# Kernel optimization log

Measured on AMD Instinct MI355X. Metric: run time of the kernel, lower is better.

## Reference

```python
import jax, jax.numpy as jnp
import numpy as np
import math

HIDDEN, HEADS, D_K = 768, 12, 64
BS, SEQ = 4, 2048


def setup_inputs() -> dict:
    key = jax.random.key(0)
    ks = jax.random.split(key, 5)
    s = 1.0 / math.sqrt(HIDDEN)
    return {
        "x": jax.random.normal(ks[0], (BS, SEQ, HIDDEN), dtype=jnp.float32),
        "Wq": jax.random.normal(ks[1], (HIDDEN, HIDDEN), dtype=jnp.float32) * s,
        "bq": jnp.zeros((HIDDEN,), jnp.float32),
        "Wk": jax.random.normal(ks[2], (HIDDEN, HIDDEN), dtype=jnp.float32) * s,
        "bk": jnp.zeros((HIDDEN,), jnp.float32),
        "Wv": jax.random.normal(ks[3], (HIDDEN, HIDDEN), dtype=jnp.float32) * s,
        "bv": jnp.zeros((HIDDEN,), jnp.float32),
        "Wo": jax.random.normal(ks[4], (HIDDEN, HIDDEN), dtype=jnp.float32) * s,
        "bo": jnp.zeros((HIDDEN,), jnp.float32),
    }


def reference(x, Wq, bq, Wk, bk, Wv, bv, Wo, bo):
    bs, seq, _ = x.shape
    # projections; nn.Linear computes x @ W.T + b
    def proj(W, b):
        y = jnp.einsum("bsd,ed->bse", x, W) + b
        return y.reshape(bs, seq, HEADS, D_K).transpose(0, 2, 1, 3)  # [b,h,s,d]
    q, k, v = proj(Wq, bq), proj(Wk, bk), proj(Wv, bv)
    scores = jnp.einsum("bhqd,bhkd->bhqk", q, k) / jnp.sqrt(jnp.float32(D_K))
    attn = jax.nn.softmax(scores, axis=-1)  # dropout = 0 (eval)
    ctx = jnp.einsum("bhqk,bhkd->bhqd", attn, v)
    ctx = ctx.transpose(0, 2, 1, 3).reshape(bs, seq, HIDDEN)
    return jnp.einsum("bsd,ed->bse", ctx, Wo) + bo
```

## Files before the change

kernel.cpp:

```cpp
#include <hip/hip_runtime.h>
#include <hip/hip_bf16.h>

#define HID 768
#define NHEAD 12
#define DKH 64
#define BSZ 4
#define SEQ 2048
#define MTOT (BSZ*SEQ)
#define NBH (BSZ*NHEAD)

typedef __attribute__((ext_vector_type(8))) short   s16x8;
typedef __attribute__((ext_vector_type(8))) __bf16  bf16x8;
typedef __attribute__((ext_vector_type(4))) __bf16  bf16x4;
typedef __attribute__((ext_vector_type(4))) float   f32x4;

#define MFMA16x32(A,B,C) __builtin_amdgcn_mfma_f32_16x16x32_bf16((A),(B),(C),0,0,0)

__device__ __forceinline__ unsigned short f2bf(float f) {
  union { float f; unsigned int u; } a; a.f = f;
  return (unsigned short)((a.u + 0x7FFFu + ((a.u >> 16) & 1u)) >> 16);
}

__device__ __forceinline__ void gload_lds16(const unsigned short* g, unsigned short* l) {
  __builtin_amdgcn_global_load_lds((const __attribute__((address_space(1))) void*)g,
                                   (__attribute__((address_space(3))) void*)l, 16, 0, 0);
}

__global__ __launch_bounds__(256) void cvt_kernel(const float* __restrict__ src,
                                                  unsigned short* __restrict__ dst, int n) {
  int i = (blockIdx.x * 256 + threadIdx.x) * 4;
  if (i >= n) return;
  float4 v = *(const float4*)(src + i);
  ushort4 o;
  o.x = f2bf(v.x); o.y = f2bf(v.y); o.z = f2bf(v.z); o.w = f2bf(v.w);
  *(ushort4*)(dst + i) = o;
}

__global__ __launch_bounds__(256) void cvtw_kernel(const float* __restrict__ s0,
                                                   const float* __restrict__ s1,
                                                   const float* __restrict__ s2,
                                                   const float* __restrict__ s3,
                                                   unsigned short* __restrict__ dst) {
  const float* s = (blockIdx.y == 0) ? s0 : (blockIdx.y == 1) ? s1 : (blockIdx.y == 2) ? s2 : s3;
  int i = (blockIdx.x * 256 + threadIdx.x) * 4;
  float4 v = *(const float4*)(s + i);
  ushort4 o;
  o.x = f2bf(v.x); o.y = f2bf(v.y); o.z = f2bf(v.z); o.w = f2bf(v.w);
  *(ushort4*)(dst + (size_t)blockIdx.y * HID * HID + i) = o;
}

template<int MODE>
__global__ __launch_bounds__(256) void gemm_kernel(
    const unsigned short* __restrict__ A,
    const unsigned short* __restrict__ W,
    const float* __restrict__ bias0,
    const float* __restrict__ bias1,
    const float* __restrict__ bias2,
    void* __restrict__ out_raw,
    unsigned short* __restrict__ vtimg)
{
  __shared__ unsigned short As[128*64];
  __shared__ unsigned short Bs[128*64];
  const int tid  = threadIdx.x;
  const int wave = tid >> 6, lane = tid & 63;
  const int l16  = lane & 15, lg = lane >> 4;
  const int f    = blockIdx.x;
  const int xcd  = f & 7, rr = f >> 3;
  const int bx   = xcd*8 + (rr & 7), by = rr >> 3;
  const int m0   = bx * 128, n0 = by * 128;
  const int wm   = (wave & 1) * 64,  wn = (wave >> 1) * 64;

  const f32x4 z4 = {0.f, 0.f, 0.f, 0.f};
  f32x4 acc[4][4];
#pragma unroll
  for (int i = 0; i < 4; ++i)
#pragma unroll
    for (int j = 0; j < 4; ++j) acc[i][j] = z4;

  const int sr  = lane >> 3;
  const int sc8 = ((lane & 7) ^ sr) << 3;

  for (int kt = 0; kt < HID; kt += 64) {
    __syncthreads();
#pragma unroll
    for (int i = 0; i < 4; ++i) {
      const int c = wave * 4 + i;
      gload_lds16(A + (size_t)(m0 + c*8 + sr) * HID + kt + sc8, As + c*512);
      gload_lds16(W + (size_t)(n0 + c*8 + sr) * HID + kt + sc8, Bs + c*512);
    }
    __syncthreads();
    const char* ab = (const char*)As;
    const char* bb = (const char*)Bs;
#pragma unroll
    for (int kk = 0; kk < 2; ++kk) {
      bf16x8 af[4], bfr[4];
#pragma unroll
      for (int mb = 0; mb < 4; ++mb) {
        const int r = wm + mb*16 + l16;
        af[mb] = *(const bf16x8*)(ab + r*128 + (((kk*4 + lg) ^ (l16 & 7)) << 4));
      }
#pragma unroll
      for (int nb = 0; nb < 4; ++nb) {
        const int r = wn + nb*16 + l16;
        bfr[nb] = *(const bf16x8*)(bb + r*128 + (((kk*4 + lg) ^ (l16 & 7)) << 4));
      }
#pragma unroll
      for (int mb = 0; mb < 4; ++mb)
#pragma unroll
        for (int nb = 0; nb < 4; ++nb)
          acc[mb][nb] = MFMA16x32(af[mb], bfr[nb], acc[mb][nb]);
    }
  }

  if (MODE == 0) {
    unsigned short* out = (unsigned short*)out_raw;
    const float QSCALE = 0.18033688011112042f;
    const int which = (n0 + wn) / HID;
    if (which == 2) {
      const int h = (n0 + wn - 2*HID) >> 6;
#pragma unroll
      for (int nb = 0; nb < 4; ++nb) {
        const int d = nb*16 + l16;
        const float bias = bias2[h*64 + d];
#pragma unroll
        for (int mb = 0; mb < 4; ++mb) {
          const int m    = m0 + wm + mb*16 + lg*4;
          const int b    = m >> 11, s = m & (SEQ - 1);
          const int tile = s >> 6;
          const int slot = ((s & 63) >> 2) ^ l16;
          ushort4 w;
          w.x = f2bf(acc[mb][nb][0] + bias);
          w.y = f2bf(acc[mb][nb][1] + bias);
          w.z = f2bf(acc[mb][nb][2] + bias);
          w.w = f2bf(acc[mb][nb][3] + bias);
          *(ushort4*)(vtimg + ((((size_t)(b*NHEAD + h)*32 + tile)*64 + d)*64 + slot*4)) = w;
        }
      }
    } else {
      const float* bp  = (which == 0) ? bias0 : bias1;
      const float scl  = (which == 0) ? QSCALE : 1.0f;
      const int e_base = n0 + wn - which*HID;
#pragma unroll
      for (int nb = 0; nb < 4; ++nb) {
        const int e = e_base + nb*16 + l16;
        const float bias = bp[e];
        const int h = e >> 6, d = e & 63;
#pragma unroll
        for (int mb = 0; mb < 4; ++mb)
#pragma unroll
          for (int j = 0; j < 4; ++j) {
            const int m = m0 + wm + mb*16 + lg*4 + j;
            const int b = m >> 11, s = m & (SEQ - 1);
            const float v = (acc[mb][nb][j] + bias) * scl;
            out[((((size_t)which*BSZ + b)*NHEAD + h)*SEQ + s)*DKH + d] = f2bf(v);
          }
      }
    }
  } else {
    float* out = (float*)out_raw;
#pragma unroll
    for (int nb = 0; nb < 4; ++nb) {
      const int n = n0 + wn + nb*16 + l16;
      const float bias = bias0[n];
#pragma unroll
      for (int mb = 0; mb < 4; ++mb)
#pragma unroll
        for (int j = 0; j < 4; ++j) {
          const int m = m0 + wm + mb*16 + lg*4 + j;
          out[(size_t)m*HID + n] = acc[mb][nb][j] + bias;
        }
    }
  }
}

#define ATTN_STEP(CUR, DOPREF)                                              \
  {                                                                         \
    if (DOPREF) {                                                           \
      gload_lds16(kSrc0, Ks[(CUR)^1] + wave*1024);                          \
      gload_lds16(kSrc1, Ks[(CUR)^1] + wave*1024 + 512);                    \
      gload_lds16(vSrc0, Vs[(CUR)^1] + wave*1024);                          \
      gload_lds16(vSrc1, Vs[(CUR)^1] + wave*1024 + 512);                    \
      kSrc0 += 64*DKH; kSrc1 += 64*DKH; vSrc0 += 4096; vSrc1 += 4096;       \
    }                                                                       \
    const char* kb = (const char*)Ks[CUR];                                  \
    const char* vb = (const char*)Vs[CUR];                                  \
    f32x4 sc[2][4];                                                         \
    __builtin_amdgcn_s_setprio(1);                                          \
    _Pragma("unroll")                                                       \
    for (int nb = 0; nb < 4; ++nb) {                                        \
      bf16x8 kf0 = *(const bf16x8*)(kb + kbase0 + nb*2048);                 \
      bf16x8 kf1 = *(const bf16x8*)(kb + kbase1 + nb*2048);                 \
      f32x4 z0 = z4, z1 = z4;                                               \
      z0 = MFMA16x32(kf0, qf[0][0], z0);                                    \
      z0 = MFMA16x32(kf1, qf[0][1], z0);                                    \
      z1 = MFMA16x32(kf0, qf[1][0], z1);                                    \
      z1 = MFMA16x32(kf1, qf[1][1], z1);                                    \
      sc[0][nb] = z0; sc[1][nb] = z1;                                       \
    }                                                                       \
    __builtin_amdgcn_s_setprio(0);                                          \
    bf16x8 pa[2][2];                                                        \
    _Pragma("unroll")                                                       \
    for (int qa = 0; qa < 2; ++qa)                                          \
      _Pragma("unroll")                                                     \
      for (int nb = 0; nb < 4; ++nb)                                        \
        _Pragma("unroll")                                                   \
        for (int j = 0; j < 4; ++j)                                         \
          pa[qa][nb>>1][(nb&1)*4 + j] =                                     \
            (__bf16)__builtin_amdgcn_exp2f(sc[qa][nb][j]);                  \
    __builtin_amdgcn_s_setprio(1);                                          \
    csum[0] = MFMA16x32(pa[0][0], ones, csum[0]);                           \
    csum[0] = MFMA16x32(pa[0][1], ones, csum[0]);                           \
    csum[1] = MFMA16x32(pa[1][0], ones, csum[1]);                           \
    csum[1] = MFMA16x32(pa[1][1], ones, csum[1]);                           \
    _Pragma("unroll")                                                       \
    for (int db = 0; db < 4; ++db) {                                        \
      bf16x4 v00 = *(const bf16x4*)(vb + vbase0 + db*2048);                 \
      bf16x4 v01 = *(const bf16x4*)(vb + vbase1 + db*2048);                 \
      bf16x4 v10 = *(const bf16x4*)(vb + vbase2 + db*2048);                 \
      bf16x4 v11 = *(const bf16x4*)(vb + vbase3 + db*2048);                 \
      bf16x8 vf0 = __builtin_shufflevector(v00, v01, 0,1,2,3,4,5,6,7);      \
      bf16x8 vf1 = __builtin_shufflevector(v10, v11, 0,1,2,3,4,5,6,7);      \
      cacc[0][db] = MFMA16x32(pa[0][0], vf0, cacc[0][db]);                  \
      cacc[0][db] = MFMA16x32(pa[0][1], vf1, cacc[0][db]);                  \
      cacc[1][db] = MFMA16x32(pa[1][0], vf0, cacc[1][db]);                  \
      cacc[1][db] = MFMA16x32(pa[1][1], vf1, cacc[1][db]);                  \
    }                                                                       \
    __builtin_amdgcn_s_setprio(0);                                          \
    __syncthreads();                                                        \
  }

__global__ __launch_bounds__(256, 3) void attn_kernel(const unsigned short* __restrict__ qkv,
                                                      const unsigned short* __restrict__ vtimg,
                                                      unsigned short* __restrict__ ctx)
{
  __shared__ unsigned short Ks[2][64*64];
  __shared__ unsigned short Vs[2][64*64];
  const int tid  = threadIdx.x;
  const int wave = tid >> 6, lane = tid & 63;
  const int l16  = lane & 15, lg = lane >> 4;
  const int f   = blockIdx.x;
  const int xcd = f & 7, idx = f >> 3;
  const int bh  = xcd * 6 + (idx >> 4);
  const int qt  = idx & 15;
  const int b   = bh / NHEAD, h = bh - b * NHEAD;
  const int q0  = qt * 128 + wave * 32;

  const unsigned short* Qg = qkv + (size_t)bh * (SEQ*DKH);
  const unsigned short* Kg = qkv + (size_t)(NBH + bh) * (SEQ*DKH);

  const int srow  = lane >> 3;
  const int scolK = ((lane & 7) ^ srow) << 3;
  const unsigned short* kSrc0 = Kg + (size_t)(wave*16 + srow) * DKH + scolK;
  const unsigned short* kSrc1 = Kg + (size_t)(wave*16 + 8 + srow) * DKH + scolK;
  const unsigned short* vSrc0 = vtimg + ((size_t)bh*32*64 + wave*16 + srow) * 64 + (lane & 7) * 8;
  const unsigned short* vSrc1 = vSrc0 + 8*64;

  const int kbase0 = l16*128 + ((lg ^ (l16 & 7)) << 4);
  const int kbase1 = l16*128 + (((lg + 4) ^ (l16 & 7)) << 4);
  const int vbase0 = l16*128 + (((lg     ) ^ l16) << 3);
  const int vbase1 = l16*128 + (((lg +  4) ^ l16) << 3);
  const int vbase2 = l16*128 + (((lg +  8) ^ l16) << 3);
  const int vbase3 = l16*128 + (((lg + 12) ^ l16) << 3);

  bf16x8 qf[2][2];
#pragma unroll
  for (int qa = 0; qa < 2; ++qa) {
    qf[qa][0] = *(const bf16x8*)(Qg + (size_t)(q0 + qa*16 + l16)*DKH + lg*8);
    qf[qa][1] = *(const bf16x8*)(Qg + (size_t)(q0 + qa*16 + l16)*DKH + 32 + lg*8);
  }

  bf16x8 ones;
#pragma unroll
  for (int e = 0; e < 8; ++e) ones[e] = (__bf16)1.0f;

  const f32x4 z4 = {0.f,0.f,0.f,0.f};
  f32x4 cacc[2][4];
  f32x4 csum[2] = {z4, z4};
#pragma unroll
  for (int qa = 0; qa < 2; ++qa)
#pragma unroll
    for (int db = 0; db < 4; ++db) cacc[qa][db] = z4;

  gload_lds16(kSrc0, Ks[0] + wave*1024);
  gload_lds16(kSrc1, Ks[0] + wave*1024 + 512);
  gload_lds16(vSrc0, Vs[0] + wave*1024);
  gload_lds16(vSrc1, Vs[0] + wave*1024 + 512);
  kSrc0 += 64*DKH; kSrc1 += 64*DKH; vSrc0 += 4096; vSrc1 += 4096;
  __syncthreads();

#pragma unroll 1
  for (int tt = 0; tt < 16; ++tt) {
    ATTN_STEP(0, true)
    ATTN_STEP(1, (tt < 15))
  }

#pragma unroll
  for (int qa = 0; qa < 2; ++qa) {
    f32x4 inv;
#pragma unroll
    for (int j = 0; j < 4; ++j) inv[j] = 1.0f / csum[qa][j];
#pragma unroll
    for (int db = 0; db < 4; ++db)
#pragma unroll
      for (int j = 0; j < 4; ++j) {
        const int srow2 = q0 + qa*16 + lg*4 + j;
        ctx[((size_t)(b*SEQ + srow2))*HID + h*DKH + db*16 + l16] = f2bf(cacc[qa][db][j] * inv[j]);
      }
  }
}

extern "C" void kernel_launch(void* const* d_in, const int* in_sizes, int n_in,
                              void* d_out, int out_size, void* d_ws, size_t ws_size,
                              hipStream_t stream) {
  (void)in_sizes; (void)n_in; (void)out_size; (void)ws_size;
  const float* x  = (const float*)d_in[0];
  const float* Wq = (const float*)d_in[1];
  const float* bq = (const float*)d_in[2];
  const float* Wk = (const float*)d_in[3];
  const float* bk = (const float*)d_in[4];
  const float* Wv = (const float*)d_in[5];
  const float* bv = (const float*)d_in[6];
  const float* Wo = (const float*)d_in[7];
  const float* bo = (const float*)d_in[8];

  unsigned short* ws   = (unsigned short*)d_ws;
  unsigned short* Xb   = ws;
  unsigned short* Wqkv = Xb + (size_t)MTOT * HID;
  unsigned short* Wob  = Wqkv + (size_t)3 * HID * HID;
  unsigned short* qkvb = Wob + (size_t)HID * HID;
  unsigned short* vtb  = qkvb + (size_t)2 * NBH * SEQ * DKH;
  unsigned short* ctxb = Xb;

  cvt_kernel<<<(MTOT*HID)/1024, 256, 0, stream>>>(x, Xb, MTOT*HID);
  cvtw_kernel<<<dim3((HID*HID)/1024, 4), 256, 0, stream>>>(Wq, Wk, Wv, Wo, Wqkv);

  gemm_kernel<0><<<1152, 256, 0, stream>>>(Xb, Wqkv, bq, bk, bv, qkvb, vtb);
  attn_kernel<<<768, 256, 0, stream>>>(qkvb, vtb, ctxb);
  gemm_kernel<1><<<384, 256, 0, stream>>>(ctxb, Wob, bo, nullptr, nullptr, d_out, nullptr);
}
```

Before: 135.3 us.

## Double-buffer GEMM LDS tiles to overlap global loads with MFMA compute

The GEMM kernel now keeps two LDS buffers for the A and W tiles. It issues the global-to-LDS loads for the next K tile before computing on the current one, with one barrier per step instead of two. This is meant to hide global memory latency behind MFMA work. The cost is doubled LDS use (64KB per block), which may reduce occupancy. Correctness also depends on the global_load_lds completing before the barrier that follows.

```diff
diff --git a/kernel.cpp b/kernel.cpp
--- a/kernel.cpp
+++ b/kernel.cpp
@@ -49,6 +49,42 @@
   *(ushort4*)(dst + (size_t)blockIdx.y * HID * HID + i) = o;
 }
 
+#define GEMM_STEP(CUR, KTN, DOPREF)                                         \
+  {                                                                         \
+    if (DOPREF) {                                                           \
+      _Pragma("unroll")                                                     \
+      for (int i = 0; i < 4; ++i) {                                         \
+        const int c = wave * 4 + i;                                         \
+        gload_lds16(Aptr + (size_t)(c*8 + sr) * HID + (KTN) + sc8,          \
+                    As[(CUR)^1] + c*512);                                   \
+        gload_lds16(Wptr + (size_t)(c*8 + sr) * HID + (KTN) + sc8,          \
+                    Bs[(CUR)^1] + c*512);                                   \
+      }                                                                     \
+    }                                                                       \
+    const char* ab = (const char*)As[CUR];                                  \
+    const char* bb = (const char*)Bs[CUR];                                  \
+    _Pragma("unroll")                                                       \
+    for (int kk = 0; kk < 2; ++kk) {                                        \
+      bf16x8 af[4], bfr[4];                                                 \
+      _Pragma("unroll")                                                     \
+      for (int mb = 0; mb < 4; ++mb) {                                      \
+        const int r = wm + mb*16 + l16;                                     \
+        af[mb] = *(const bf16x8*)(ab + r*128 + (((kk*4 + lg) ^ (l16 & 7)) << 4)); \
+      }                                                                     \
+      _Pragma("unroll")                                                     \
+      for (int nb = 0; nb < 4; ++nb) {                                      \
+        const int r = wn + nb*16 + l16;                                     \
+        bfr[nb] = *(const bf16x8*)(bb + r*128 + (((kk*4 + lg) ^ (l16 & 7)) << 4)); \
+      }                                                                     \
+      _Pragma("unroll")                                                     \
+      for (int mb = 0; mb < 4; ++mb)                                        \
+        _Pragma("unroll")                                                   \
+        for (int nb = 0; nb < 4; ++nb)                                      \
+          acc[mb][nb] = MFMA16x32(af[mb], bfr[nb], acc[mb][nb]);            \
+    }                                                                       \
+    __syncthreads();                                                        \
+  }
+
 template<int MODE>
 __global__ __launch_bounds__(256) void gemm_kernel(
     const unsigned short* __restrict__ A,
@@ -59,8 +95,8 @@
     void* __restrict__ out_raw,
     unsigned short* __restrict__ vtimg)
 {
-  __shared__ unsigned short As[128*64];
-  __shared__ unsigned short Bs[128*64];
+  __shared__ unsigned short As[2][128*64];
+  __shared__ unsigned short Bs[2][128*64];
   const int tid  = threadIdx.x;
   const int wave = tid >> 6, lane = tid & 63;
   const int l16  = lane & 15, lg = lane >> 4;
@@ -79,37 +115,21 @@
 
   const int sr  = lane >> 3;
   const int sc8 = ((lane & 7) ^ sr) << 3;
-
-  for (int kt = 0; kt < HID; kt += 64) {
-    __syncthreads();
-#pragma unroll
-    for (int i = 0; i < 4; ++i) {
-      const int c = wave * 4 + i;
-      gload_lds16(A + (size_t)(m0 + c*8 + sr) * HID + kt + sc8, As + c*512);
-      gload_lds16(W + (size_t)(n0 + c*8 + sr) * HID + kt + sc8, Bs + c*512);
-    }
-    __syncthreads();
-    const char* ab = (const char*)As;
-    const char* bb = (const char*)Bs;
-#pragma unroll
-    for (int kk = 0; kk < 2; ++kk) {
-      bf16x8 af[4], bfr[4];
-#pragma unroll
-      for (int mb = 0; mb < 4; ++mb) {
-        const int r = wm + mb*16 + l16;
-        af[mb] = *(const bf16x8*)(ab + r*128 + (((kk*4 + lg) ^ (l16 & 7)) << 4));
-      }
-#pragma unroll
-      for (int nb = 0; nb < 4; ++nb) {
-        const int r = wn + nb*16 + l16;
-        bfr[nb] = *(const bf16x8*)(bb + r*128 + (((kk*4 + lg) ^ (l16 & 7)) << 4));
-      }
-#pragma unroll
-      for (int mb = 0; mb < 4; ++mb)
-#pragma unroll
-        for (int nb = 0; nb < 4; ++nb)
-          acc[mb][nb] = MFMA16x32(af[mb], bfr[nb], acc[mb][nb]);
-    }
+  const unsigned short* Aptr = A + (size_t)m0 * HID;
+  const unsigned short* Wptr = W + (size_t)n0 * HID;
+
+#pragma unroll
+  for (int i = 0; i < 4; ++i) {
+    const int c = wave * 4 + i;
+    gload_lds16(Aptr + (size_t)(c*8 + sr) * HID + sc8, As[0] + c*512);
+    gload_lds16(Wptr + (size_t)(c*8 + sr) * HID + sc8, Bs[0] + c*512);
+  }
+  __syncthreads();
+
+#pragma unroll 1
+  for (int tt = 0; tt < 6; ++tt) {
+    GEMM_STEP(0, (2*tt+1)*64, true)
+    GEMM_STEP(1, (2*tt+2)*64, (tt < 5))
   }
 
   if (MODE == 0) {
```

New measurement: 130.8 us. 3.4% less time.
